# Kernel tuning notes

Measured on AMD Instinct MI355X. Metric: run time of the kernel, lower is better.

The kernel has to match this reference:

```python
import jax, jax.numpy as jnp
import numpy as np

N = 50000
E = 800000
G_DIM = 512
H1 = 128
H2 = 128
R = 8  # 2 * n_speakers**2


def setup_inputs() -> dict:
    key = jax.random.key(0)
    ks = jax.random.split(key, 16)
    s = lambda d: 1.0 / np.sqrt(d)
    inp = {
        'node_features': jax.random.normal(ks[0], (N, G_DIM), jnp.float32),
        'edge_index': jax.random.randint(ks[1], (2, E), 0, N, jnp.int64),
        'edge_type': jax.random.randint(ks[2], (E,), 0, R, jnp.int64),
        # RGCNConv params
        'W_rel': jax.random.normal(ks[3], (R, G_DIM, H1), jnp.float32) * s(G_DIM),
        'W_root': jax.random.normal(ks[4], (G_DIM, H1), jnp.float32) * s(G_DIM),
        'b1': jnp.zeros((H1,), jnp.float32),
        # TransformerConv params (heads=1)
        'Wq': jax.random.normal(ks[5], (H1, H2), jnp.float32) * s(H1),
        'bq': jnp.zeros((H2,), jnp.float32),
        'Wk': jax.random.normal(ks[6], (H1, H2), jnp.float32) * s(H1),
        'bk': jnp.zeros((H2,), jnp.float32),
        'Wv': jax.random.normal(ks[7], (H1, H2), jnp.float32) * s(H1),
        'bv': jnp.zeros((H2,), jnp.float32),
        'Wskip': jax.random.normal(ks[8], (H1, H2), jnp.float32) * s(H1),
        'bskip': jnp.zeros((H2,), jnp.float32),
        # BatchNorm1d params
        'gamma': jnp.ones((H2,), jnp.float32),
        'beta': jnp.zeros((H2,), jnp.float32),
    }
    return inp


def reference(node_features, edge_index, edge_type, W_rel, W_root, b1,
              Wq, bq, Wk, bk, Wv, bv, Wskip, bskip, gamma, beta):
    n = node_features.shape[0]
    r = W_rel.shape[0]
    src, dst = edge_index[0], edge_index[1]

    # ---- RGCNConv: per-relation mean aggregation + root + bias ----
    # x @ W_r for all relations, then per-edge gather: [n,r,h1] -> [E,h1]
    xW = jnp.einsum('nf,rfh->nrh', node_features, W_rel)
    msg = xW[src, edge_type]                         # [E, H1]
    comp = dst * r + edge_type                       # composite (node, relation) key
    cnt = jax.ops.segment_sum(jnp.ones((msg.shape[0],), msg.dtype), comp,
                              num_segments=n * r)
    denom = jnp.maximum(cnt[comp], 1.0)[:, None]     # mean within each (node, rel)
    agg1 = jax.ops.segment_sum(msg / denom, dst, num_segments=n)
    h = agg1 + node_features @ W_root + b1           # [n, H1]

    # ---- TransformerConv (heads=1): segment-softmax attention ----
    q = h @ Wq + bq
    k = h @ Wk + bk
    v = h @ Wv + bv
    d = q.shape[-1]
    score = jnp.sum(q[dst] * k[src], axis=-1) / jnp.sqrt(jnp.float32(d))  # [E]
    smax = jax.ops.segment_max(score, dst, num_segments=n)
    smax = jnp.where(jnp.isfinite(smax), smax, 0.0)
    ex = jnp.exp(score - smax[dst])
    ssum = jax.ops.segment_sum(ex, dst, num_segments=n)
    alpha = ex / jnp.maximum(ssum[dst], 1e-16)       # [E]
    agg2 = jax.ops.segment_sum(alpha[:, None] * v[src], dst, num_segments=n)
    h2 = agg2 + h @ Wskip + bskip                    # root (lin_skip) path

    # ---- BatchNorm1d (training mode: batch stats) + LeakyReLU(0.01) ----
    mu = jnp.mean(h2, axis=0)
    var = jnp.mean((h2 - mu) ** 2, axis=0)
    xn = (h2 - mu) / jnp.sqrt(var + 1e-5)
    out = gamma * xn + beta
    return jnp.where(out >= 0, out, 0.01 * out)
```

## Files before the change

kernel.cpp:

```cpp
#include <hip/hip_runtime.h>

typedef float f32x4 __attribute__((ext_vector_type(4)));
typedef _Float16 f16x8 __attribute__((ext_vector_type(8)));

#define NN 50000
#define EE 800000
#define GD 512
#define H1C 128
#define RR 8
#define NC1 1152
#define NC2 512
#define SCAN_BLK 256

__device__ __forceinline__ unsigned short f2h(float f){
  _Float16 h = (_Float16)f;
  unsigned short u; __builtin_memcpy(&u, &h, 2); return u;
}
__device__ __forceinline__ float h2f(unsigned short u){
  _Float16 h; __builtin_memcpy(&h, &u, 2); return (float)h;
}
__device__ __forceinline__ void gload16(const void* g, void* l){
  __builtin_amdgcn_global_load_lds(
      (const __attribute__((address_space(1))) unsigned int*)g,
      (__attribute__((address_space(3))) unsigned int*)l, 16, 0, 0);
}

__global__ void k_fill_u32(unsigned* p, unsigned v, int n){
  int i = blockIdx.x * blockDim.x + threadIdx.x;
  if (i < n) p[i] = v;
}

__global__ void k_cast_f16(const float* __restrict__ in, unsigned short* __restrict__ out, int n){
  int i = (blockIdx.x * blockDim.x + threadIdx.x) * 4;
  if (i + 3 < n){
    float4 v = *(const float4*)(in + i);
    ushort4 o;
    o.x = f2h(v.x); o.y = f2h(v.y); o.z = f2h(v.z); o.w = f2h(v.w);
    *(ushort4*)(out + i) = o;
  }
}

__global__ void k_pack_w1(const float* __restrict__ W_rel, const float* __restrict__ W_root,
                          unsigned short* __restrict__ wcatT){
  int idx = blockIdx.x * blockDim.x + threadIdx.x;
  if (idx >= NC1 * GD) return;
  int j = idx >> 9;
  int f = idx & 511;
  float v;
  if (j < 1024) v = W_rel[((size_t)(j >> 7) * GD + f) * H1C + (j & 127)];
  else          v = W_root[(size_t)f * H1C + (j - 1024)];
  wcatT[(size_t)j * GD + f] = f2h(v);
}

__global__ void k_pack_w2(const float* __restrict__ Wq, const float* __restrict__ Wk,
                          const float* __restrict__ Wv, const float* __restrict__ Ws,
                          const float* __restrict__ bq, const float* __restrict__ bk,
                          const float* __restrict__ bv, const float* __restrict__ bs,
                          unsigned short* __restrict__ w2T, float* __restrict__ bias2){
  int idx = blockIdx.x * blockDim.x + threadIdx.x;
  if (idx >= NC2 * H1C) return;
  int j = idx >> 7;
  int f = idx & 127;
  int m = j >> 7;
  int hc = j & 127;
  const float* W = (m == 0) ? Wq : (m == 1) ? Wk : (m == 2) ? Wv : Ws;
  w2T[(size_t)j * H1C + f] = f2h(W[(size_t)f * H1C + hc]);
  if (f == 0){
    const float* B = (m == 0) ? bq : (m == 1) ? bk : (m == 2) ? bv : bs;
    bias2[j] = B[hc];
  }
}

__global__ void k_hist(const int* __restrict__ ei, const int* __restrict__ et,
                       int* __restrict__ deg, float* __restrict__ cnt, int E){
  int e = blockIdx.x * blockDim.x + threadIdx.x;
  if (e >= E) return;
  int dst = ei[E + e];
  atomicAdd(&deg[dst], 1);
  atomicAdd(&cnt[(size_t)dst * RR + et[e]], 1.0f);
}

__global__ void k_scan_partial(const int* __restrict__ deg, int* __restrict__ bsum, int n){
  __shared__ int s[SCAN_BLK];
  int i = blockIdx.x * SCAN_BLK + threadIdx.x;
  s[threadIdx.x] = (i < n) ? deg[i] : 0;
  __syncthreads();
  for (int off = 128; off >= 1; off >>= 1){
    if (threadIdx.x < off) s[threadIdx.x] += s[threadIdx.x + off];
    __syncthreads();
  }
  if (threadIdx.x == 0) bsum[blockIdx.x] = s[0];
}

__global__ void k_scan_top(int* __restrict__ bsum, int* __restrict__ boff, int nb){
  __shared__ int s[SCAN_BLK];
  int t = threadIdx.x;
  int v = (t < nb) ? bsum[t] : 0;
  s[t] = v;
  __syncthreads();
  #pragma unroll
  for (int off = 1; off < SCAN_BLK; off <<= 1){
    int tv = (t >= off) ? s[t - off] : 0;
    __syncthreads();
    s[t] += tv;
    __syncthreads();
  }
  if (t < nb) boff[t] = s[t] - v;
}

__global__ void k_scan_final(const int* __restrict__ deg, const int* __restrict__ boff,
                             int* __restrict__ base, int n){
  __shared__ int s[SCAN_BLK];
  int i = blockIdx.x * SCAN_BLK + threadIdx.x;
  int t = threadIdx.x;
  int v = (i < n) ? deg[i] : 0;
  s[t] = v;
  __syncthreads();
  #pragma unroll
  for (int off = 1; off < SCAN_BLK; off <<= 1){
    int tv = (t >= off) ? s[t - off] : 0;
    __syncthreads();
    s[t] += tv;
    __syncthreads();
  }
  if (i < n) base[i] = s[t] - v + boff[blockIdx.x];
}

__global__ void k_scatter_perm(const int* __restrict__ ei, const int* __restrict__ et,
                               const int* __restrict__ base, int* __restrict__ cursor,
                               unsigned* __restrict__ sortedSR, int E){
  int e = blockIdx.x * blockDim.x + threadIdx.x;
  if (e >= E) return;
  int dst = ei[E + e];
  int pos = base[dst] + atomicAdd(&cursor[dst], 1);
  sortedSR[pos] = (unsigned)(ei[e] & 0xFFFF) | ((unsigned)et[e] << 16);
}

#define TILE 128
#define BK 64

__global__ __launch_bounds__(256) void k_gemm(
    const unsigned short* __restrict__ A,
    const unsigned short* __restrict__ Bt,
    unsigned short* __restrict__ C,
    const float* __restrict__ bias,
    int M, int Nout, int K, int rowsPerXcd, int colBlocks)
{
  int bid = blockIdx.x;
  int xcd = bid & 7;
  int lin = bid >> 3;
  int rowb = xcd * rowsPerXcd + lin / colBlocks;
  int colb = lin % colBlocks;
  int row0 = rowb * TILE;
  if (row0 >= M) return;
  int col0 = colb * TILE;

  __shared__ unsigned short As[TILE][BK];
  __shared__ unsigned short Bs[TILE][BK];
  int tid = threadIdx.x;
  int wave = tid >> 6, lane = tid & 63;
  int wm = (wave >> 1) * 64, wn = (wave & 1) * 64;
  int l16 = lane & 15, quad = lane >> 4;

  int srow = lane >> 3;
  int gcb  = ((lane & 7) ^ srow) * 8;
  int xorr = l16 & 7;

  f32x4 acc[4][4] = {};

  for (int k0 = 0; k0 < K; k0 += BK){
    __syncthreads();
    #pragma unroll
    for (int i = 0; i < 4; i++){
      int rbase = (wave * 4 + i) * 8;
      int gr = row0 + rbase + srow; if (gr >= M) gr = M - 1;
      gload16(A + (size_t)gr * K + k0 + gcb, &As[rbase][0]);
    }
    #pragma unroll
    for (int i = 0; i < 4; i++){
      int rbase = (wave * 4 + i) * 8;
      int gc = col0 + rbase + srow;
      gload16(Bt + (size_t)gc * K + k0 + gcb, &Bs[rbase][0]);
    }
    __syncthreads();
    #pragma unroll
    for (int ks = 0; ks < BK; ks += 32){
      int scol = ((quad + (ks >> 3)) ^ xorr) * 8;
      f16x8 af[4], bfr[4];
      #pragma unroll
      for (int i = 0; i < 4; i++) af[i] = *(const f16x8*)&As[wm + i*16 + l16][scol];
      #pragma unroll
      for (int j = 0; j < 4; j++) bfr[j] = *(const f16x8*)&Bs[wn + j*16 + l16][scol];
      #pragma unroll
      for (int i = 0; i < 4; i++)
        #pragma unroll
        for (int j = 0; j < 4; j++)
          acc[i][j] = __builtin_amdgcn_mfma_f32_16x16x32_f16(af[i], bfr[j], acc[i][j], 0, 0, 0);
    }
  }

  #pragma unroll
  for (int i = 0; i < 4; i++){
    int rbase = row0 + wm + i*16 + quad*4;
    #pragma unroll
    for (int j = 0; j < 4; j++){
      int col = col0 + wn + j*16 + l16;
      float b = bias ? bias[col] : 0.0f;
      #pragma unroll
      for (int rr = 0; rr < 4; rr++){
        int row = rbase + rr;
        if (row < M) C[(size_t)row * Nout + col] = f2h(acc[i][j][rr] + b);
      }
    }
  }
}

__global__ __launch_bounds__(256) void k_rgcn_seg(
    const int* __restrict__ base, const int* __restrict__ deg,
    const unsigned* __restrict__ srt,
    const unsigned short* __restrict__ xW, const float* __restrict__ cnt,
    const float* __restrict__ b1, unsigned short* __restrict__ h16)
{
  int v = blockIdx.x * 4 + (threadIdx.x >> 6);
  if (v >= NN) return;
  int lane = threadIdx.x & 63;
  int g = lane >> 4, l16 = lane & 15;
  int start = base[v], d = deg[v];
  const float* cv = cnt + (size_t)v * RR;

  float o[8] = {};
  for (int cb = 0; cb < d; cb += 4){
    int idx = cb + g;
    bool valid = idx < d;
    unsigned sri = valid ? srt[start + idx] : 0u;
    int src = (int)(sri & 0xFFFFu);
    int rel = (int)(sri >> 16);
    float inv = valid ? 1.0f / fmaxf(cv[rel], 1.0f) : 0.0f;
    uint4 u = *(const uint4*)(xW + (size_t)src * NC1 + rel * H1C + l16 * 8);
    const unsigned short* p = (const unsigned short*)&u;
    #pragma unroll
    for (int j = 0; j < 8; j++) o[j] += h2f(p[j]) * inv;
  }
  #pragma unroll
  for (int j = 0; j < 8; j++){
    o[j] += __shfl_xor(o[j], 16, 64);
    o[j] += __shfl_xor(o[j], 32, 64);
  }
  if (g == 0){
    uint4 r = *(const uint4*)(xW + (size_t)v * NC1 + 1024 + l16 * 8);
    const unsigned short* p = (const unsigned short*)&r;
    unsigned short res[8];
    #pragma unroll
    for (int j = 0; j < 8; j++) res[j] = f2h(o[j] + h2f(p[j]) + b1[l16 * 8 + j]);
    *(uint4*)(h16 + (size_t)v * H1C + l16 * 8) = *(uint4*)res;
  }
}

__global__ __launch_bounds__(256) void k_attn3(
    const int* __restrict__ base, const int* __restrict__ deg,
    const unsigned* __restrict__ srt,
    const unsigned short* __restrict__ qkvs, float* __restrict__ h2)
{
  int v = blockIdx.x * 4 + (threadIdx.x >> 6);
  if (v >= NN) return;
  int lane = threadIdx.x & 63;
  int g = lane >> 4, l16 = lane & 15;
  int start = base[v], d = deg[v];
  const float sc = 0.08838834764831845f;

  float qf[8];
  {
    uint4 qa = *(const uint4*)(qkvs + (size_t)v * NC2 + l16 * 8);
    const unsigned short* p = (const unsigned short*)&qa;
    #pragma unroll
    for (int i = 0; i < 8; i++) qf[i] = h2f(p[i]);
  }

  float o[8] = {};
  float m = -INFINITY, l = 0.0f;

  for (int cb = 0; cb < d; cb += 4){
    int idx = cb + g;
    bool valid = idx < d;
    int src = valid ? (int)(srt[start + idx] & 0xFFFFu) : 0;

    float ss = 0.0f;
    {
      uint4 ka = *(const uint4*)(qkvs + (size_t)src * NC2 + 128 + l16 * 8);
      const unsigned short* p = (const unsigned short*)&ka;
      #pragma unroll
      for (int i = 0; i < 8; i++) ss += qf[i] * h2f(p[i]);
      #pragma unroll
      for (int off = 8; off >= 1; off >>= 1) ss += __shfl_xor(ss, off, 16);
    }
    float s = valid ? ss * sc : -INFINITY;

    float m4 = s;
    m4 = fmaxf(m4, __shfl_xor(m4, 16, 64));
    m4 = fmaxf(m4, __shfl_xor(m4, 32, 64));
    float newm = fmaxf(m, m4);
    float scale = __expf(m - newm);
    float e = valid ? __expf(s - newm) : 0.0f;
    float esum = e;
    esum += __shfl_xor(esum, 16, 64);
    esum += __shfl_xor(esum, 32, 64);
    l = l * scale + esum;

    uint4 va = *(const uint4*)(qkvs + (size_t)src * NC2 + 256 + l16 * 8);
    const unsigned short* p = (const unsigned short*)&va;
    #pragma unroll
    for (int j = 0; j < 8; j++) o[j] = o[j] * scale + e * h2f(p[j]);
    m = newm;
  }

  #pragma unroll
  for (int j = 0; j < 8; j++){
    o[j] += __shfl_xor(o[j], 16, 64);
    o[j] += __shfl_xor(o[j], 32, 64);
  }
  if (g == 0){
    float r = (d > 0) ? 1.0f / fmaxf(l, 1e-16f) : 0.0f;
    uint4 sk = *(const uint4*)(qkvs + (size_t)v * NC2 + 384 + l16 * 8);
    const unsigned short* p = (const unsigned short*)&sk;
    float* hd = h2 + (size_t)v * H1C + l16 * 8;
    float4 r0 = make_float4(h2f(p[0]) + o[0]*r, h2f(p[1]) + o[1]*r,
                            h2f(p[2]) + o[2]*r, h2f(p[3]) + o[3]*r);
    float4 r1 = make_float4(h2f(p[4]) + o[4]*r, h2f(p[5]) + o[5]*r,
                            h2f(p[6]) + o[6]*r, h2f(p[7]) + o[7]*r);
    *(float4*)hd = r0;
    *(float4*)(hd + 4) = r1;
  }
}

__global__ __launch_bounds__(256) void k_bn_reduce(const float* __restrict__ h2,
                                                   float* __restrict__ bn, int Nrows){
  __shared__ float ls[256], lq[256];
  int c = threadIdx.x & 127;
  int half = threadIdx.x >> 7;
  float s = 0.0f, q = 0.0f;
  for (int r = blockIdx.x * 2 + half; r < Nrows; r += gridDim.x * 2){
    float v = h2[(size_t)r * H1C + c];
    s += v; q += v * v;
  }
  ls[threadIdx.x] = s; lq[threadIdx.x] = q;
  __syncthreads();
  if (half == 0){
    atomicAdd(&bn[c],        ls[c] + ls[c + 128]);
    atomicAdd(&bn[128 + c],  lq[c] + lq[c + 128]);
  }
}

__global__ void k_bn_final(float* __restrict__ bn, int Nrows){
  int c = threadIdx.x;
  if (c >= 128) return;
  float mu = bn[c] / (float)Nrows;
  float var = bn[128 + c] / (float)Nrows - mu * mu;
  bn[256 + c] = mu;
  bn[384 + c] = rsqrtf(var + 1e-5f);
}

__global__ void k_out(const float* __restrict__ h2, const float* __restrict__ bn,
                      const float* __restrict__ gamma, const float* __restrict__ beta,
                      float* __restrict__ out, int n){
  int idx = blockIdx.x * blockDim.x + threadIdx.x;
  if (idx >= n) return;
  int c = idx & 127;
  float v = (h2[idx] - bn[256 + c]) * bn[384 + c];
  float o = gamma[c] * v + beta[c];
  out[idx] = (o >= 0.0f) ? o : 0.01f * o;
}

extern "C" void kernel_launch(void* const* d_in, const int* in_sizes, int n_in,
                              void* d_out, int out_size, void* d_ws, size_t ws_size,
                              hipStream_t stream) {
  const float* x      = (const float*)d_in[0];
  const int*   ei     = (const int*)d_in[1];
  const int*   et     = (const int*)d_in[2];
  const float* W_rel  = (const float*)d_in[3];
  const float* W_root = (const float*)d_in[4];
  const float* b1     = (const float*)d_in[5];
  const float* Wq     = (const float*)d_in[6];
  const float* bq     = (const float*)d_in[7];
  const float* Wk     = (const float*)d_in[8];
  const float* bk     = (const float*)d_in[9];
  const float* Wv     = (const float*)d_in[10];
  const float* bv     = (const float*)d_in[11];
  const float* Wskip  = (const float*)d_in[12];
  const float* bskip  = (const float*)d_in[13];
  const float* gamma  = (const float*)d_in[14];
  const float* beta   = (const float*)d_in[15];
  float* out = (float*)d_out;

  const int N = NN, E = EE;
  char* ws = (char*)d_ws;
  size_t off = 0;
  auto alloc = [&](size_t bytes){ size_t r = off; off = (off + bytes + 255) & ~(size_t)255; return r; };

  size_t o_x16   = alloc((size_t)N * GD * 2);
  size_t o_w1    = alloc((size_t)NC1 * GD * 2);
  size_t o_xw    = alloc((size_t)N * NC1 * 2);
  size_t o_cnt   = alloc((size_t)N * RR * 4);
  size_t o_deg   = alloc((size_t)N * 4);
  size_t o_cur   = alloc((size_t)N * 4);
  size_t o_zend  = off;
  size_t o_base  = alloc((size_t)N * 4);
  size_t o_bsum  = alloc((size_t)SCAN_BLK * 4);
  size_t o_boff  = alloc((size_t)SCAN_BLK * 4);
  size_t o_srt   = alloc((size_t)E * 4);
  size_t o_h16   = alloc((size_t)N * H1C * 2);
  size_t o_w2    = alloc((size_t)NC2 * H1C * 2);
  size_t o_b2    = alloc((size_t)NC2 * 4);
  size_t o_bn    = alloc((size_t)512 * 4);

  unsigned short* x16   = (unsigned short*)(ws + o_x16);
  unsigned short* qkvs  = (unsigned short*)(ws + o_x16);
  unsigned short* wcatT = (unsigned short*)(ws + o_w1);
  unsigned short* xW    = (unsigned short*)(ws + o_xw);
  float*          h2    = (float*)(ws + o_xw);
  float*          cnt   = (float*)(ws + o_cnt);
  int*            deg   = (int*)(ws + o_deg);
  int*            cursor= (int*)(ws + o_cur);
  int*            basea = (int*)(ws + o_base);
  int*            bsum  = (int*)(ws + o_bsum);
  int*            boff  = (int*)(ws + o_boff);
  unsigned*       srt   = (unsigned*)(ws + o_srt);
  unsigned short* h16   = (unsigned short*)(ws + o_h16);
  unsigned short* w2T   = (unsigned short*)(ws + o_w2);
  float*          bias2 = (float*)(ws + o_b2);
  float*          bn    = (float*)(ws + o_bn);

  const int TPB = 256;
  const int NBLK = (N + SCAN_BLK - 1) / SCAN_BLK;
  const int ROWB = (N + TILE - 1) / TILE;
  const int RPX  = (ROWB + 7) / 8;

  int nzero = (int)((o_zend - o_cnt) / 4);
  k_fill_u32<<<(nzero + TPB - 1) / TPB, TPB, 0, stream>>>((unsigned*)(ws + o_cnt), 0u, nzero);
  k_hist<<<(E + TPB - 1) / TPB, TPB, 0, stream>>>(ei, et, deg, cnt, E);
  k_scan_partial<<<NBLK, SCAN_BLK, 0, stream>>>(deg, bsum, N);
  k_scan_top<<<1, SCAN_BLK, 0, stream>>>(bsum, boff, NBLK);
  k_scan_final<<<NBLK, SCAN_BLK, 0, stream>>>(deg, boff, basea, N);
  k_scatter_perm<<<(E + TPB - 1) / TPB, TPB, 0, stream>>>(ei, et, basea, cursor, srt, E);

  k_cast_f16<<<((size_t)N * GD / 4 + TPB - 1) / TPB, TPB, 0, stream>>>(x, x16, N * GD);
  k_pack_w1<<<(NC1 * GD + TPB - 1) / TPB, TPB, 0, stream>>>(W_rel, W_root, wcatT);
  k_gemm<<<8 * RPX * (NC1 / TILE), TPB, 0, stream>>>(x16, wcatT, xW, nullptr, N, NC1, GD, RPX, NC1 / TILE);

  k_rgcn_seg<<<(N + 3) / 4, TPB, 0, stream>>>(basea, deg, srt, xW, cnt, b1, h16);

  k_pack_w2<<<(NC2 * H1C + TPB - 1) / TPB, TPB, 0, stream>>>(Wq, Wk, Wv, Wskip, bq, bk, bv, bskip, w2T, bias2);
  k_gemm<<<8 * RPX * (NC2 / TILE), TPB, 0, stream>>>(h16, w2T, qkvs, bias2, N, NC2, H1C, RPX, NC2 / TILE);

  k_attn3<<<(N + 3) / 4, TPB, 0, stream>>>(basea, deg, srt, qkvs, h2);

  k_fill_u32<<<2, 256, 0, stream>>>((unsigned*)bn, 0u, 512);
  k_bn_reduce<<<256, TPB, 0, stream>>>(h2, bn, N);
  k_bn_final<<<1, 128, 0, stream>>>(bn, N);
  k_out<<<((size_t)N * H1C + TPB - 1) / TPB, TPB, 0, stream>>>(h2, bn, gamma, beta, out, N * H1C);
}
```

Measured before the change: 620.4 us.

## Merge prep kernels, derive degree from counts, batch edge gathers by four

```diff
diff --git a/kernel.cpp b/kernel.cpp
--- a/kernel.cpp
+++ b/kernel.cpp
@@ -11,6 +11,7 @@
 #define NC1 1152
 #define NC2 512
 #define SCAN_BLK 256
+#define NCAST (NN * GD / 4)
 
 __device__ __forceinline__ unsigned short f2h(float f){
   _Float16 h = (_Float16)f;
@@ -25,65 +26,71 @@
       (__attribute__((address_space(3))) unsigned int*)l, 16, 0, 0);
 }
 
-__global__ void k_fill_u32(unsigned* p, unsigned v, int n){
-  int i = blockIdx.x * blockDim.x + threadIdx.x;
-  if (i < n) p[i] = v;
-}
-
-__global__ void k_cast_f16(const float* __restrict__ in, unsigned short* __restrict__ out, int n){
-  int i = (blockIdx.x * blockDim.x + threadIdx.x) * 4;
-  if (i + 3 < n){
-    float4 v = *(const float4*)(in + i);
+__global__ void k_prep(unsigned* __restrict__ zp, int nzero,
+                       const float* __restrict__ x, unsigned short* __restrict__ x16,
+                       const float* __restrict__ W_rel, const float* __restrict__ W_root,
+                       unsigned short* __restrict__ wcatT,
+                       const float* __restrict__ Wq, const float* __restrict__ Wk,
+                       const float* __restrict__ Wv, const float* __restrict__ Ws,
+                       const float* __restrict__ bq, const float* __restrict__ bk,
+                       const float* __restrict__ bv, const float* __restrict__ bs,
+                       unsigned short* __restrict__ w2T, float* __restrict__ bias2){
+  int i = blockIdx.x * 256 + threadIdx.x;
+  if (i < nzero){ zp[i] = 0u; return; }
+  i -= nzero;
+  if (i < NCAST){
+    int b = i * 4;
+    float4 v = *(const float4*)(x + b);
     ushort4 o;
     o.x = f2h(v.x); o.y = f2h(v.y); o.z = f2h(v.z); o.w = f2h(v.w);
-    *(ushort4*)(out + i) = o;
-  }
-}
-
-__global__ void k_pack_w1(const float* __restrict__ W_rel, const float* __restrict__ W_root,
-                          unsigned short* __restrict__ wcatT){
-  int idx = blockIdx.x * blockDim.x + threadIdx.x;
-  if (idx >= NC1 * GD) return;
-  int j = idx >> 9;
-  int f = idx & 511;
-  float v;
-  if (j < 1024) v = W_rel[((size_t)(j >> 7) * GD + f) * H1C + (j & 127)];
-  else          v = W_root[(size_t)f * H1C + (j - 1024)];
-  wcatT[(size_t)j * GD + f] = f2h(v);
-}
-
-__global__ void k_pack_w2(const float* __restrict__ Wq, const float* __restrict__ Wk,
-                          const float* __restrict__ Wv, const float* __restrict__ Ws,
-                          const float* __restrict__ bq, const float* __restrict__ bk,
-                          const float* __restrict__ bv, const float* __restrict__ bs,
-                          unsigned short* __restrict__ w2T, float* __restrict__ bias2){
-  int idx = blockIdx.x * blockDim.x + threadIdx.x;
-  if (idx >= NC2 * H1C) return;
-  int j = idx >> 7;
-  int f = idx & 127;
-  int m = j >> 7;
-  int hc = j & 127;
-  const float* W = (m == 0) ? Wq : (m == 1) ? Wk : (m == 2) ? Wv : Ws;
-  w2T[(size_t)j * H1C + f] = f2h(W[(size_t)f * H1C + hc]);
-  if (f == 0){
-    const float* B = (m == 0) ? bq : (m == 1) ? bk : (m == 2) ? bv : bs;
-    bias2[j] = B[hc];
+    *(ushort4*)(x16 + b) = o;
+    return;
+  }
+  i -= NCAST;
+  if (i < NC1 * GD){
+    int j = i >> 9;
+    int f = i & 511;
+    float v;
+    if (j < 1024) v = W_rel[((size_t)(j >> 7) * GD + f) * H1C + (j & 127)];
+    else          v = W_root[(size_t)f * H1C + (j - 1024)];
+    wcatT[(size_t)j * GD + f] = f2h(v);
+    return;
+  }
+  i -= NC1 * GD;
+  if (i < NC2 * H1C){
+    int j = i >> 7;
+    int f = i & 127;
+    int m = j >> 7;
+    int hc = j & 127;
+    const float* W = (m == 0) ? Wq : (m == 1) ? Wk : (m == 2) ? Wv : Ws;
+    w2T[(size_t)j * H1C + f] = f2h(W[(size_t)f * H1C + hc]);
+    if (f == 0){
+      const float* B = (m == 0) ? bq : (m == 1) ? bk : (m == 2) ? bv : bs;
+      bias2[j] = B[hc];
+    }
   }
 }
 
 __global__ void k_hist(const int* __restrict__ ei, const int* __restrict__ et,
-                       int* __restrict__ deg, float* __restrict__ cnt, int E){
+                       float* __restrict__ cnt, int E){
   int e = blockIdx.x * blockDim.x + threadIdx.x;
   if (e >= E) return;
-  int dst = ei[E + e];
-  atomicAdd(&deg[dst], 1);
-  atomicAdd(&cnt[(size_t)dst * RR + et[e]], 1.0f);
-}
-
-__global__ void k_scan_partial(const int* __restrict__ deg, int* __restrict__ bsum, int n){
+  atomicAdd(&cnt[(size_t)ei[E + e] * RR + et[e]], 1.0f);
+}
+
+__global__ void k_scan_partial(const float* __restrict__ cnt, int* __restrict__ deg,
+                               int* __restrict__ bsum, int n){
   __shared__ int s[SCAN_BLK];
   int i = blockIdx.x * SCAN_BLK + threadIdx.x;
-  s[threadIdx.x] = (i < n) ? deg[i] : 0;
+  int dv = 0;
+  if (i < n){
+    const float4* c = (const float4*)(cnt + (size_t)i * 8);
+    float4 a = c[0], b = c[1];
+    float fs = a.x + a.y + a.z + a.w + b.x + b.y + b.z + b.w;
+    dv = (int)(fs + 0.5f);
+    deg[i] = dv;
+  }
+  s[threadIdx.x] = dv;
   __syncthreads();
   for (int off = 128; off >= 1; off >>= 1){
     if (threadIdx.x < off) s[threadIdx.x] += s[threadIdx.x + off];
@@ -229,17 +236,27 @@
   const float* cv = cnt + (size_t)v * RR;
 
   float o[8] = {};
-  for (int cb = 0; cb < d; cb += 4){
-    int idx = cb + g;
-    bool valid = idx < d;
-    unsigned sri = valid ? srt[start + idx] : 0u;
-    int src = (int)(sri & 0xFFFFu);
-    int rel = (int)(sri >> 16);
-    float inv = valid ? 1.0f / fmaxf(cv[rel], 1.0f) : 0.0f;
-    uint4 u = *(const uint4*)(xW + (size_t)src * NC1 + rel * H1C + l16 * 8);
-    const unsigned short* p = (const unsigned short*)&u;
-    #pragma unroll
-    for (int j = 0; j < 8; j++) o[j] += h2f(p[j]) * inv;
+  for (int cb = 0; cb < d; cb += 16){
+    int srcs[4]; int rels[4]; float invs[4];
+    #pragma unroll
+    for (int t = 0; t < 4; t++){
+      int idx = cb + 4 * t + g;
+      bool valid = idx < d;
+      unsigned sri = valid ? srt[start + idx] : 0u;
+      srcs[t] = (int)(sri & 0xFFFFu);
+      rels[t] = (int)(sri >> 16);
+      invs[t] = valid ? 1.0f / fmaxf(cv[rels[t]], 1.0f) : 0.0f;
+    }
+    uint4 u[4];
+    #pragma unroll
+    for (int t = 0; t < 4; t++)
+      u[t] = *(const uint4*)(xW + (size_t)srcs[t] * NC1 + rels[t] * H1C + l16 * 8);
+    #pragma unroll
+    for (int t = 0; t < 4; t++){
+      const unsigned short* p = (const unsigned short*)&u[t];
+      #pragma unroll
+      for (int j = 0; j < 8; j++) o[j] += h2f(p[j]) * invs[t];
+    }
   }
   #pragma unroll
   for (int j = 0; j < 8; j++){
@@ -279,37 +296,57 @@
   float o[8] = {};
   float m = -INFINITY, l = 0.0f;
 
-  for (int cb = 0; cb < d; cb += 4){
-    int idx = cb + g;
-    bool valid = idx < d;
-    int src = valid ? (int)(srt[start + idx] & 0xFFFFu) : 0;
-
-    float ss = 0.0f;
-    {
-      uint4 ka = *(const uint4*)(qkvs + (size_t)src * NC2 + 128 + l16 * 8);
-      const unsigned short* p = (const unsigned short*)&ka;
+  for (int cb = 0; cb < d; cb += 16){
+    int srcs[4]; bool val[4];
+    #pragma unroll
+    for (int t = 0; t < 4; t++){
+      int idx = cb + 4 * t + g;
+      val[t] = idx < d;
+      srcs[t] = val[t] ? (int)(srt[start + idx] & 0xFFFFu) : 0;
+    }
+    uint4 ka[4], va[4];
+    #pragma unroll
+    for (int t = 0; t < 4; t++)
+      ka[t] = *(const uint4*)(qkvs + (size_t)srcs[t] * NC2 + 128 + l16 * 8);
+    #pragma unroll
+    for (int t = 0; t < 4; t++)
+      va[t] = *(const uint4*)(qkvs + (size_t)srcs[t] * NC2 + 256 + l16 * 8);
+
+    float s[4];
+    #pragma unroll
+    for (int t = 0; t < 4; t++){
+      const unsigned short* p = (const unsigned short*)&ka[t];
+      float ss = 0.0f;
       #pragma unroll
       for (int i = 0; i < 8; i++) ss += qf[i] * h2f(p[i]);
       #pragma unroll
       for (int off = 8; off >= 1; off >>= 1) ss += __shfl_xor(ss, off, 16);
-    }
-    float s = valid ? ss * sc : -INFINITY;
-
-    float m4 = s;
+      s[t] = val[t] ? ss * sc : -INFINITY;
+    }
+
+    float m4 = fmaxf(fmaxf(s[0], s[1]), fmaxf(s[2], s[3]));
     m4 = fmaxf(m4, __shfl_xor(m4, 16, 64));
     m4 = fmaxf(m4, __shfl_xor(m4, 32, 64));
     float newm = fmaxf(m, m4);
     float scale = __expf(m - newm);
-    float e = valid ? __expf(s - newm) : 0.0f;
-    float esum = e;
+    float e[4], esum = 0.0f;
+    #pragma unroll
+    for (int t = 0; t < 4; t++){
+      e[t] = val[t] ? __expf(s[t] - newm) : 0.0f;
+      esum += e[t];
+    }
     esum += __shfl_xor(esum, 16, 64);
     esum += __shfl_xor(esum, 32, 64);
     l = l * scale + esum;
 
-    uint4 va = *(const uint4*)(qkvs + (size_t)src * NC2 + 256 + l16 * 8);
-    const unsigned short* p = (const unsigned short*)&va;
-    #pragma unroll
-    for (int j = 0; j < 8; j++) o[j] = o[j] * scale + e * h2f(p[j]);
+    #pragma unroll
+    for (int j = 0; j < 8; j++) o[j] *= scale;
+    #pragma unroll
+    for (int t = 0; t < 4; t++){
+      const unsigned short* p = (const unsigned short*)&va[t];
+      #pragma unroll
+      for (int j = 0; j < 8; j++) o[j] += e[t] * h2f(p[j]);
+    }
     m = newm;
   }
 
@@ -350,22 +387,16 @@
   }
 }
 
-__global__ void k_bn_final(float* __restrict__ bn, int Nrows){
-  int c = threadIdx.x;
-  if (c >= 128) return;
-  float mu = bn[c] / (float)Nrows;
-  float var = bn[128 + c] / (float)Nrows - mu * mu;
-  bn[256 + c] = mu;
-  bn[384 + c] = rsqrtf(var + 1e-5f);
-}
-
 __global__ void k_out(const float* __restrict__ h2, const float* __restrict__ bn,
                       const float* __restrict__ gamma, const float* __restrict__ beta,
-                      float* __restrict__ out, int n){
+                      float* __restrict__ out, int n, float invN){
   int idx = blockIdx.x * blockDim.x + threadIdx.x;
   if (idx >= n) return;
   int c = idx & 127;
-  float v = (h2[idx] - bn[256 + c]) * bn[384 + c];
+  float mu = bn[c] * invN;
+  float var = bn[128 + c] * invN - mu * mu;
+  float rs = rsqrtf(var + 1e-5f);
+  float v = (h2[idx] - mu) * rs;
   float o = gamma[c] * v + beta[c];
   out[idx] = (o >= 0.0f) ? o : 0.01f * o;
 }
@@ -400,9 +431,10 @@
   size_t o_w1    = alloc((size_t)NC1 * GD * 2);
   size_t o_xw    = alloc((size_t)N * NC1 * 2);
   size_t o_cnt   = alloc((size_t)N * RR * 4);
+  size_t o_cur   = alloc((size_t)N * 4);
+  size_t o_bn    = alloc((size_t)512 * 4);
+  size_t o_zend  = off;
   size_t o_deg   = alloc((size_t)N * 4);
-  size_t o_cur   = alloc((size_t)N * 4);
-  size_t o_zend  = off;
   size_t o_base  = alloc((size_t)N * 4);
   size_t o_bsum  = alloc((size_t)SCAN_BLK * 4);
   size_t o_boff  = alloc((size_t)SCAN_BLK * 4);
@@ -410,7 +442,6 @@
   size_t o_h16   = alloc((size_t)N * H1C * 2);
   size_t o_w2    = alloc((size_t)NC2 * H1C * 2);
   size_t o_b2    = alloc((size_t)NC2 * 4);
-  size_t o_bn    = alloc((size_t)512 * 4);
 
   unsigned short* x16   = (unsigned short*)(ws + o_x16);
   unsigned short* qkvs  = (unsigned short*)(ws + o_x16);
@@ -418,8 +449,9 @@
   unsigned short* xW    = (unsigned short*)(ws + o_xw);
   float*          h2    = (float*)(ws + o_xw);
   float*          cnt   = (float*)(ws + o_cnt);
+  int*            cursor= (int*)(ws + o_cur);
+  float*          bn    = (float*)(ws + o_bn);
   int*            deg   = (int*)(ws + o_deg);
-  int*            cursor= (int*)(ws + o_cur);
   int*            basea = (int*)(ws + o_base);
   int*            bsum  = (int*)(ws + o_bsum);
   int*            boff  = (int*)(ws + o_boff);
@@ -427,7 +459,6 @@
   unsigned short* h16   = (unsigned short*)(ws + o_h16);
   unsigned short* w2T   = (unsigned short*)(ws + o_w2);
   float*          bias2 = (float*)(ws + o_b2);
-  float*          bn    = (float*)(ws + o_bn);
 
   const int TPB = 256;
   const int NBLK = (N + SCAN_BLK - 1) / SCAN_BLK;
@@ -435,26 +466,25 @@
   const int RPX  = (ROWB + 7) / 8;
 
   int nzero = (int)((o_zend - o_cnt) / 4);
-  k_fill_u32<<<(nzero + TPB - 1) / TPB, TPB, 0, stream>>>((unsigned*)(ws + o_cnt), 0u, nzero);
-  k_hist<<<(E + TPB - 1) / TPB, TPB, 0, stream>>>(ei, et, deg, cnt, E);
-  k_scan_partial<<<NBLK, SCAN_BLK, 0, stream>>>(deg, bsum, N);
+  long prepN = (long)nzero + NCAST + NC1 * GD + NC2 * H1C;
+  k_prep<<<(prepN + TPB - 1) / TPB, TPB, 0, stream>>>(
+      (unsigned*)(ws + o_cnt), nzero, x, x16, W_rel, W_root, wcatT,
+      Wq, Wk, Wv, Wskip, bq, bk, bv, bskip, w2T, bias2);
+
+  k_hist<<<(E + TPB - 1) / TPB, TPB, 0, stream>>>(ei, et, cnt, E);
+  k_scan_partial<<<NBLK, SCAN_BLK, 0, stream>>>(cnt, deg, bsum, N);
   k_scan_top<<<1, SCAN_BLK, 0, stream>>>(bsum, boff, NBLK);
   k_scan_final<<<NBLK, SCAN_BLK, 0, stream>>>(deg, boff, basea, N);
   k_scatter_perm<<<(E + TPB - 1) / TPB, TPB, 0, stream>>>(ei, et, basea, cursor, srt, E);
 
-  k_cast_f16<<<((size_t)N * GD / 4 + TPB - 1) / TPB, TPB, 0, stream>>>(x, x16, N * GD);
-  k_pack_w1<<<(NC1 * GD + TPB - 1) / TPB, TPB, 0, stream>>>(W_rel, W_root, wcatT);
   k_gemm<<<8 * RPX * (NC1 / TILE), TPB, 0, stream>>>(x16, wcatT, xW, nullptr, N, NC1, GD, RPX, NC1 / TILE);
 
   k_rgcn_seg<<<(N + 3) / 4, TPB, 0, stream>>>(basea, deg, srt, xW, cnt, b1, h16);
 
-  k_pack_w2<<<(NC2 * H1C + TPB - 1) / TPB, TPB, 0, stream>>>(Wq, Wk, Wv, Wskip, bq, bk, bv, bskip, w2T, bias2);
   k_gemm<<<8 * RPX * (NC2 / TILE), TPB, 0, stream>>>(h16, w2T, qkvs, bias2, N, NC2, H1C, RPX, NC2 / TILE);
 
   k_attn3<<<(N + 3) / 4, TPB, 0, stream>>>(basea, deg, srt, qkvs, h2);
 
-  k_fill_u32<<<2, 256, 0, stream>>>((unsigned*)bn, 0u, 512);
   k_bn_reduce<<<256, TPB, 0, stream>>>(h2, bn, N);
-  k_bn_final<<<1, 128, 0, stream>>>(bn, N);
-  k_out<<<((size_t)N * H1C + TPB - 1) / TPB, TPB, 0, stream>>>(h2, bn, gamma, beta, out, N * H1C);
-}
+  k_out<<<((size_t)N * H1C + TPB - 1) / TPB, TPB, 0, stream>>>(h2, bn, gamma, beta, out, N * H1C, 1.0f / N);
+}
```

Measured after the change: 569.9 us. -8.1%, faster.
